# Optimization experiments

Measured on AMD Instinct MI355X. Metric: run time of the kernel, lower is better.

Reference implementation:

```python
import jax, jax.numpy as jnp
import numpy as np

B, C, H_IMG, W_IMG = 16, 384, 56, 56
NUM_HEADS = 6
HEAD_DIM = C // NUM_HEADS
BN_EPS = 1e-5


def _bn(x, gamma, beta, mean, var):
    # x: [b, ch, n] or [b, ch, h, w]; per-channel affine normalization (eval-mode BatchNorm)
    shape = (1, -1) + (1,) * (x.ndim - 2)
    scale = (gamma / jnp.sqrt(var + BN_EPS)).reshape(shape)
    shift = (beta - mean * gamma / jnp.sqrt(var + BN_EPS)).reshape(shape)
    return x * scale + shift


def setup_inputs() -> dict:
    key = jax.random.key(0)
    ks = jax.random.split(key, 12)
    c2 = 2 * C
    return {
        "x": jax.random.normal(ks[0], (B, C, H_IMG, W_IMG), jnp.float32),
        "qk_w": jax.random.normal(ks[1], (c2, C // 2), jnp.float32) * 0.05,
        "qk_gamma": jax.random.uniform(ks[2], (c2,), jnp.float32, 0.5, 1.5),
        "qk_beta": jax.random.normal(ks[3], (c2,), jnp.float32) * 0.1,
        "qk_mean": jax.random.normal(ks[4], (c2,), jnp.float32) * 0.1,
        "qk_var": jax.random.uniform(ks[5], (c2,), jnp.float32, 0.5, 1.5),
        "pe_w": jax.random.normal(ks[6], (C, 1, 3, 3), jnp.float32) * 0.1,
        "pe_gamma": jax.random.uniform(ks[7], (C,), jnp.float32, 0.5, 1.5),
        "pe_beta": jax.random.normal(ks[8], (C,), jnp.float32) * 0.1,
        "pe_mean": jax.random.normal(ks[9], (C,), jnp.float32) * 0.1,
        "pe_var": jax.random.uniform(ks[10], (C,), jnp.float32, 0.5, 1.5),
    }


def reference(x, qk_w, qk_gamma, qk_beta, qk_mean, qk_var,
              pe_w, pe_gamma, pe_beta, pe_mean, pe_var):
    b, c, h, w = x.shape
    n = h * w
    s = n ** (-0.5)
    nh, hd = NUM_HEADS, HEAD_DIM

    # grouped (groups=2) 1x1 conv: out channels [0:c] from input [0:c/2], [c:2c] from [c/2:c]
    xg = x.reshape(b, 2, c // 2, n)                       # [b, 2, c/2, n]
    wg = qk_w.reshape(2, c, c // 2)                       # [group, out_per_group, in_per_group]
    qk = jnp.einsum('bgin,goi->bgon', xg, wg).reshape(b, 2 * c, n)
    qk = _bn(qk, qk_gamma, qk_beta, qk_mean, qk_var)
    qk = jax.nn.elu(qk) + 1.0

    qk = qk.reshape(b, 2, nh, hd, n)
    q, k = qk[:, 0], qk[:, 1]                             # [b, H, d, n]
    v = x.reshape(b, nh, hd, n)                           # [b, H, d, n]

    # kv = (k*s) @ (v^T * s): [b, H, d, d]
    kv = jnp.einsum('bhdn,bhen->bhde', k * s, v * s)
    # numerator: q^T @ kv -> [b, H, n, d]
    num = jnp.einsum('bhdn,bhde->bhne', q, kv)
    # denominator: q^T @ mean_n(k) -> [b, H, n]
    den = jnp.einsum('bhdn,bhd->bhn', q, k.mean(axis=-1)) + 1e-6
    attn = (num / den[..., None]).transpose(0, 1, 3, 2).reshape(b, c, h, w)

    # depthwise 3x3 conv positional encoding on v (= x) + BN
    pe = jax.lax.conv_general_dilated(
        x, pe_w, window_strides=(1, 1), padding=((1, 1), (1, 1)),
        feature_group_count=c, dimension_numbers=('NCHW', 'OIHW', 'NCHW'))
    pe = _bn(pe, pe_gamma, pe_beta, pe_mean, pe_var)

    return attn + pe
```

## Files before the change

### kernel.cpp

```cpp
#include <hip/hip_runtime.h>
#include <math.h>

#define N_SP 3136
#define BN_EPS 1e-5f

typedef __attribute__((ext_vector_type(8))) short short8;
typedef __attribute__((ext_vector_type(4))) float f32x4;

#define K_SZ    (16*384*N_SP)
#define QB_OFF  (K_SZ)
#define QB_SZ   (16*384*N_SP)
#define KVP_OFF (QB_OFF + QB_SZ)
#define KVP_SZ  (16*6*7*64*80)
#define KVF_OFF (KVP_OFF + KVP_SZ)
#define KVF_SZ  (16*6*64*64)
#define KM_OFF  (KVF_OFF + KVF_SZ)
#define KM_SZ   (16*6*64)
#define WH_OFF  (KM_OFF + KM_SZ)
#define WSPLIT_N (2*384*192)
#define WF_G    (384*192)
#define PWS_OFF (WH_OFF + WSPLIT_N)
#define PSH_OFF (PWS_OFF + 384*9)

#define FSWZ(n) ((((n) >> 1) ^ ((n) >> 2)) & 7)

__device__ __forceinline__ void bsplit(float f, ushort& h, ushort& l) {
    uint u = __float_as_uint(f);
    uint hr = (u + 0x7FFFu + ((u >> 16) & 1u)) >> 16;
    h = (ushort)hr;
    float fh = __uint_as_float(hr << 16);
    float fl = f - fh;
    uint v = __float_as_uint(fl);
    l = (ushort)((v + 0x7FFFu + ((v >> 16) & 1u)) >> 16);
}

__global__ __launch_bounds__(256) void p0_prep(
    const float* __restrict__ qk_w, const float* __restrict__ pe_w,
    const float* __restrict__ pgamma, const float* __restrict__ pbeta,
    const float* __restrict__ pmean, const float* __restrict__ pvar,
    ushort* __restrict__ wfh, ushort* __restrict__ wfl,
    float* __restrict__ pwsc, float* __restrict__ psh)
{
    int idx = blockIdx.x * 256 + threadIdx.x;
    if (idx < WSPLIT_N) {
        int g = (idx >= WF_G) ? 1 : 0;
        int rem = idx - g * WF_G;
        int row = rem / 192, k = rem % 192;
        ushort h, l;
        bsplit(qk_w[idx], h, l);
        int dst = g * WF_G + ((row >> 4) * 24 + (k >> 3)) * 128 + (row & 15) * 8 + (k & 7);
        wfh[dst] = h;
        wfl[dst] = l;
    }
    if (idx < 384) {
        float sc = pgamma[idx] / sqrtf(pvar[idx] + BN_EPS);
        psh[idx] = pbeta[idx] - pmean[idx] * sc;
        #pragma unroll
        for (int q = 0; q < 9; ++q) pwsc[idx * 9 + q] = pe_w[idx * 9 + q] * sc;
    }
}

__global__ __launch_bounds__(256, 4) void k1_qk_mfma(
    const float* __restrict__ x, const ushort* __restrict__ wfh, const ushort* __restrict__ wfl,
    const float* __restrict__ gamma, const float* __restrict__ beta,
    const float* __restrict__ mean, const float* __restrict__ var,
    uint* __restrict__ kq, float* __restrict__ qbuf)
{
    __shared__ __align__(16) ushort Bh[4096];
    __shared__ __align__(16) ushort Bl[4096];
    __shared__ float scs[192], shs[192];

    const int bx = blockIdx.x;
    const int by = blockIdx.y;
    const int bz = blockIdx.z;
    const int b = bz >> 1, gg = bz & 1;
    const int t = threadIdx.x;
    const int lane = t & 63, wv = t >> 6;
    const int lg = lane >> 4, l15 = lane & 15;

    f32x4 acc[3][4];
    #pragma unroll
    for (int mf = 0; mf < 3; ++mf)
        #pragma unroll
        for (int nf = 0; nf < 4; ++nf)
            acc[mf][nf] = (f32x4){0.f, 0.f, 0.f, 0.f};

    const float* xg = x + (size_t)(b * 384 + gg * 192) * N_SP + bx * 64;
    const ushort* wfbh = wfh + gg * WF_G;
    const ushort* wfbl = wfl + gg * WF_G;

    for (int i = t; i < 192; i += 256) {
        int ch = gg * 384 + by * 192 + i;
        float sc = gamma[ch] / sqrtf(var[ch] + BN_EPS);
        scs[i] = sc;
        shs[i] = beta[ch] - mean[ch] * sc;
    }

    for (int kt = 0; kt < 3; ++kt) {
        #pragma unroll
        for (int li = 0; li < 2; ++li) {
            int idx = li * 256 + t;
            int kp = idx >> 4;
            int nq = idx & 15;
            int k0 = kp * 2;
            const float* px = xg + (size_t)(kt * 64 + k0) * N_SP + nq * 4;
            float4 v0 = *(const float4*)px;
            float4 v1 = *(const float4*)(px + N_SP);
            ushort h0[4], l0[4], h1[4], l1[4];
            float a0[4] = {v0.x, v0.y, v0.z, v0.w};
            float a1[4] = {v1.x, v1.y, v1.z, v1.w};
            #pragma unroll
            for (int i = 0; i < 4; ++i) { bsplit(a0[i], h0[i], l0[i]); bsplit(a1[i], h1[i], l1[i]); }
            int kb = k0 >> 3, ks = kp & 3;
            #pragma unroll
            for (int i = 0; i < 4; ++i) {
                int n = nq * 4 + i;
                int chunk = n * 8 + (kb ^ FSWZ(n));
                ((uint*)Bh)[chunk * 4 + ks] = (uint)h0[i] | ((uint)h1[i] << 16);
                ((uint*)Bl)[chunk * 4 + ks] = (uint)l0[i] | ((uint)l1[i] << 16);
            }
        }
        __syncthreads();
        #pragma unroll
        for (int s = 0; s < 2; ++s) {
            int kbq = s * 4 + lg;
            int kglob = kt * 8 + kbq;
            short8 bh[4], bl[4];
            #pragma unroll
            for (int nf = 0; nf < 4; ++nf) {
                int n = nf * 16 + l15;
                int chunk = n * 8 + (kbq ^ FSWZ(n));
                bh[nf] = *(const short8*)&Bh[chunk * 8];
                bl[nf] = *(const short8*)&Bl[chunk * 8];
            }
            #pragma unroll
            for (int mf = 0; mf < 3; ++mf) {
                int rb = by * 12 + wv * 3 + mf;
                int off = (rb * 24 + kglob) * 128 + l15 * 8;
                short8 ah = *(const short8*)&wfbh[off];
                short8 al = *(const short8*)&wfbl[off];
                #pragma unroll
                for (int nf = 0; nf < 4; ++nf) {
                    acc[mf][nf] = __builtin_amdgcn_mfma_f32_16x16x32_bf16(ah, bh[nf], acc[mf][nf], 0, 0, 0);
                    acc[mf][nf] = __builtin_amdgcn_mfma_f32_16x16x32_bf16(ah, bl[nf], acc[mf][nf], 0, 0, 0);
                    acc[mf][nf] = __builtin_amdgcn_mfma_f32_16x16x32_bf16(al, bh[nf], acc[mf][nf], 0, 0, 0);
                }
            }
        }
        __syncthreads();
    }

    size_t obase = ((size_t)b * 384 + by * 192) * N_SP + bx * 64;
    if (gg == 0) {
        #pragma unroll
        for (int mf = 0; mf < 3; ++mf)
            #pragma unroll
            for (int nf = 0; nf < 4; ++nf) {
                #pragma unroll
                for (int r = 0; r < 4; ++r) {
                    int lrow = wv * 48 + mf * 16 + lg * 4 + r;
                    float v = acc[mf][nf][r] * scs[lrow] + shs[lrow];
                    v = v > 0.f ? v + 1.f : __expf(v);
                    qbuf[obase + (size_t)lrow * N_SP + nf * 16 + l15] = v;
                }
            }
    } else {
        #pragma unroll
        for (int mf = 0; mf < 3; ++mf)
            #pragma unroll
            for (int nf = 0; nf < 4; ++nf) {
                #pragma unroll
                for (int r = 0; r < 4; ++r) {
                    int lrow = wv * 48 + mf * 16 + lg * 4 + r;
                    float v = acc[mf][nf][r] * scs[lrow] + shs[lrow];
                    v = v > 0.f ? v + 1.f : __expf(v);
                    ushort hh, ll;
                    bsplit(v, hh, ll);
                    kq[obase + (size_t)lrow * N_SP + nf * 16 + l15] = (uint)hh | ((uint)ll << 16);
                }
            }
    }
}

__global__ __launch_bounds__(256) void k2_kv_mfma(
    const float* __restrict__ x, const uint* __restrict__ kq,
    float* __restrict__ kv_part)
{
    __shared__ __align__(16) ushort Kh[4096], Kl[4096];
    __shared__ __align__(16) ushort Vh[5120], Vl[5120];

    const int chunk = blockIdx.x;
    const int h = blockIdx.y, b = blockIdx.z;
    const int t = threadIdx.x;
    const int lane = t & 63, wv = t >> 6;
    const int lg = lane >> 4, l15 = lane & 15;

    const uint* kp  = kq + (size_t)(b*384 + h*64) * N_SP;
    const float* vp = x  + (size_t)(b*384 + h*64) * N_SP;

    #pragma unroll
    for (int li = 0; li < 4; ++li) {
        int idx = li * 256 + t;
        int row = 64 + (idx >> 6), col = idx & 63;
        int off = (row * 8 + ((col >> 3) ^ (row & 7))) * 8 + (col & 7);
        Vh[off] = (row == 64) ? (ushort)0x3F80 : (ushort)0;
        Vl[off] = 0;
    }

    f32x4 acc[5];
    #pragma unroll
    for (int nf = 0; nf < 5; ++nf) acc[nf] = (f32x4){0.f, 0.f, 0.f, 0.f};

    for (int sub = 0; sub < 7; ++sub) {
        int n0 = chunk * 448 + sub * 64;
        #pragma unroll
        for (int li = 0; li < 4; ++li) {
            int idx = li * 256 + t;
            int row = idx >> 4, sc = idx & 15;
            int off = (row * 8 + ((sc >> 1) ^ (row & 7))) * 8 + (sc & 1) * 4;
            uint4 kf = *(const uint4*)&kp[(size_t)row * N_SP + n0 + sc * 4];
            ((uint*)&Kh[off])[0] = (kf.x & 0xFFFFu) | (kf.y << 16);
            ((uint*)&Kh[off])[1] = (kf.z & 0xFFFFu) | (kf.w << 16);
            ((uint*)&Kl[off])[0] = (kf.x >> 16) | (kf.y & 0xFFFF0000u);
            ((uint*)&Kl[off])[1] = (kf.z >> 16) | (kf.w & 0xFFFF0000u);
            float4 vf = *(const float4*)&vp[(size_t)row * N_SP + n0 + sc * 4];
            ushort h0,h1,h2,h3,l0,l1,l2,l3;
            bsplit(vf.x,h0,l0); bsplit(vf.y,h1,l1); bsplit(vf.z,h2,l2); bsplit(vf.w,h3,l3);
            ((uint*)&Vh[off])[0] = (uint)h0 | ((uint)h1 << 16);
            ((uint*)&Vh[off])[1] = (uint)h2 | ((uint)h3 << 16);
            ((uint*)&Vl[off])[0] = (uint)l0 | ((uint)l1 << 16);
            ((uint*)&Vl[off])[1] = (uint)l2 | ((uint)l3 << 16);
        }
        __syncthreads();
        #pragma unroll
        for (int s = 0; s < 2; ++s) {
            int arow = wv * 16 + l15;
            int akb = (s * 4 + lg) ^ (arow & 7);
            short8 ah = *(const short8*)&Kh[(arow * 8 + akb) * 8];
            short8 al = *(const short8*)&Kl[(arow * 8 + akb) * 8];
            #pragma unroll
            for (int nf = 0; nf < 5; ++nf) {
                int brow = nf * 16 + l15;
                int bkb = (s * 4 + lg) ^ (brow & 7);
                short8 bh = *(const short8*)&Vh[(brow * 8 + bkb) * 8];
                short8 bl = *(const short8*)&Vl[(brow * 8 + bkb) * 8];
                acc[nf] = __builtin_amdgcn_mfma_f32_16x16x32_bf16(ah, bh, acc[nf], 0, 0, 0);
                acc[nf] = __builtin_amdgcn_mfma_f32_16x16x32_bf16(ah, bl, acc[nf], 0, 0, 0);
                acc[nf] = __builtin_amdgcn_mfma_f32_16x16x32_bf16(al, bh, acc[nf], 0, 0, 0);
            }
        }
        __syncthreads();
    }

    size_t base = (size_t)((b*6 + h)*7 + chunk) * 64 * 80;
    #pragma unroll
    for (int nf = 0; nf < 5; ++nf)
        #pragma unroll
        for (int r = 0; r < 4; ++r) {
            int d = wv * 16 + lg * 4 + r;
            kv_part[base + (size_t)d * 80 + nf * 16 + l15] = acc[nf][r];
        }
}

__global__ __launch_bounds__(256) void k2b_reduce(
    const float* __restrict__ kv_part,
    float* __restrict__ kvf, float* __restrict__ km)
{
    const int bh = blockIdx.x;
    const int t = threadIdx.x;
    const float inv_n = 1.0f / (float)N_SP;
    const float* base = kv_part + (size_t)bh * 7 * 5120;
    float s[20];
    #pragma unroll
    for (int j = 0; j < 20; ++j) s[j] = 0.f;
    for (int c = 0; c < 7; ++c) {
        #pragma unroll
        for (int j = 0; j < 20; ++j) s[j] += base[c * 5120 + j * 256 + t];
    }
    #pragma unroll
    for (int j = 0; j < 20; ++j) {
        int i = j * 256 + t;
        int d = i / 80, e = i % 80;
        float v = s[j] * inv_n;
        if (e < 64)       kvf[(size_t)bh * 4096 + d * 64 + e] = v;
        else if (e == 64) km[bh * 64 + d] = v;
    }
}

__global__ __launch_bounds__(256) void k3_attn_pe(
    const float* __restrict__ x, const float* __restrict__ qbuf,
    const float* __restrict__ kvf, const float* __restrict__ km,
    const float* __restrict__ pwsc, const float* __restrict__ psh,
    float* __restrict__ out)
{
    __shared__ float qs[64][68];
    __shared__ float kms[64];
    const int bx = blockIdx.x;
    const int h = blockIdx.y, b = blockIdx.z;
    const int t = threadIdx.x, tx = t & 15, ty = t >> 4;
    const int n0 = bx * 64;
    const float* qp  = qbuf + (size_t)(b * 384 + h * 64) * N_SP;
    const float* kvp = kvf + (size_t)(b * 6 + h) * 4096;
    #pragma unroll
    for (int l = 0; l < 4; ++l) {
        int idx = t + l * 256;
        int d = idx >> 4, c = idx & 15;
        *(float4*)&qs[d][c * 4] = *(const float4*)&qp[(size_t)d * N_SP + n0 + c * 4];
    }
    if (t < 64) kms[t] = km[(b * 6 + h) * 64 + t];
    __syncthreads();

    float acc[4][4] = {};
    float den[4] = {};
    #pragma unroll 8
    for (int d = 0; d < 64; ++d) {
        float4 qn = *(const float4*)&qs[d][tx * 4];
        float4 ke = *(const float4*)&kvp[d * 64 + ty * 4];
        float qq[4] = {qn.x, qn.y, qn.z, qn.w}, kk[4] = {ke.x, ke.y, ke.z, ke.w};
        float kmd = kms[d];
        #pragma unroll
        for (int p = 0; p < 4; ++p) {
            den[p] += qq[p] * kmd;
            #pragma unroll
            for (int j = 0; j < 4; ++j) acc[p][j] += qq[p] * kk[j];
        }
    }

    const int p0 = n0 + tx * 4;
    const int y = p0 / 56, xc = p0 % 56;
    #pragma unroll
    for (int j = 0; j < 4; ++j) {
        int c = h * 64 + ty * 4 + j;
        const float* xp = x + ((size_t)b * 384 + c) * N_SP;
        float s6[3][6];
        #pragma unroll
        for (int dy = 0; dy < 3; ++dy) {
            int yy = y + dy - 1;
            bool yok = (yy >= 0) && (yy < 56);
            float4 mid = make_float4(0.f, 0.f, 0.f, 0.f);
            float lf = 0.f, rt = 0.f;
            if (yok) {
                const float* xr = xp + yy * 56;
                mid = *(const float4*)&xr[xc];
                if (xc > 0)  lf = xr[xc - 1];
                if (xc < 52) rt = xr[xc + 4];
            }
            s6[dy][0] = lf;  s6[dy][1] = mid.x; s6[dy][2] = mid.y;
            s6[dy][3] = mid.z; s6[dy][4] = mid.w; s6[dy][5] = rt;
        }
        float w9[9];
        #pragma unroll
        for (int q = 0; q < 9; ++q) w9[q] = pwsc[c * 9 + q];
        float sh2 = psh[c];
        float4 r;
        float* pr = (float*)&r;
        #pragma unroll
        for (int p = 0; p < 4; ++p) {
            float conv = 0.f;
            #pragma unroll
            for (int dy = 0; dy < 3; ++dy)
                #pragma unroll
                for (int dx = 0; dx < 3; ++dx)
                    conv += w9[dy * 3 + dx] * s6[dy][p + dx];
            pr[p] = acc[p][j] / (den[p] + 1e-6f) + conv + sh2;
        }
        *(float4*)&out[((size_t)b * 384 + c) * N_SP + p0] = r;
    }
}

extern "C" void kernel_launch(void* const* d_in, const int* in_sizes, int n_in,
                              void* d_out, int out_size, void* d_ws, size_t ws_size,
                              hipStream_t stream)
{
    const float* x        = (const float*)d_in[0];
    const float* qk_w     = (const float*)d_in[1];
    const float* qk_gamma = (const float*)d_in[2];
    const float* qk_beta  = (const float*)d_in[3];
    const float* qk_mean  = (const float*)d_in[4];
    const float* qk_var   = (const float*)d_in[5];
    const float* pe_w     = (const float*)d_in[6];
    const float* pe_gamma = (const float*)d_in[7];
    const float* pe_beta  = (const float*)d_in[8];
    const float* pe_mean  = (const float*)d_in[9];
    const float* pe_var   = (const float*)d_in[10];
    float* out = (float*)d_out;

    float* ws      = (float*)d_ws;
    uint* kq       = (uint*)ws;
    float* qbuf    = ws + QB_OFF;
    float* kv_part = ws + KVP_OFF;
    float* kvf     = ws + KVF_OFF;
    float* km      = ws + KM_OFF;
    ushort* wfh    = (ushort*)(ws + WH_OFF);
    ushort* wfl    = wfh + WSPLIT_N;
    float* pwsc    = ws + PWS_OFF;
    float* psh     = ws + PSH_OFF;

    hipLaunchKernelGGL(p0_prep, dim3((WSPLIT_N + 255)/256), dim3(256), 0, stream,
                       qk_w, pe_w, pe_gamma, pe_beta, pe_mean, pe_var,
                       wfh, wfl, pwsc, psh);
    dim3 g1(49, 2, 32);
    hipLaunchKernelGGL(k1_qk_mfma, g1, dim3(256), 0, stream,
                       x, wfh, wfl, qk_gamma, qk_beta, qk_mean, qk_var, kq, qbuf);
    dim3 g2(7, 6, 16);
    hipLaunchKernelGGL(k2_kv_mfma, g2, dim3(256), 0, stream, x, kq, kv_part);
    hipLaunchKernelGGL(k2b_reduce, dim3(96), dim3(256), 0, stream,
                       kv_part, kvf, km);
    dim3 g3(49, 6, 16);
    hipLaunchKernelGGL(k3_attn_pe, g3, dim3(256), 0, stream,
                       x, qbuf, kvf, km, pwsc, psh, out);
}
```

Baseline: 215.6 us.

## Fuse Q projection into attention kernel, dropping the Q intermediate buffer

The Q half of the grouped 1x1 conv is no longer computed in k1 and written to a global fp32 buffer. k3 now recomputes Q per tile with split-bf16 MFMAs, applies BN and ELU+1 into the shared tile, and then runs the attention and positional-encoding math. This removes a 77MB write and reread of Q. It adds x loads and MFMA work inside k3, and the shared tile is reused as staging space. The BN scale and shift for Q are precomputed in the prep kernel.

```diff
diff --git a/kernel.cpp b/kernel.cpp
--- a/kernel.cpp
+++ b/kernel.cpp
@@ -8,9 +8,7 @@
 typedef __attribute__((ext_vector_type(4))) float f32x4;
 
 #define K_SZ    (16*384*N_SP)
-#define QB_OFF  (K_SZ)
-#define QB_SZ   (16*384*N_SP)
-#define KVP_OFF (QB_OFF + QB_SZ)
+#define KVP_OFF (K_SZ)
 #define KVP_SZ  (16*6*7*64*80)
 #define KVF_OFF (KVP_OFF + KVP_SZ)
 #define KVF_SZ  (16*6*64*64)
@@ -21,6 +19,8 @@
 #define WF_G    (384*192)
 #define PWS_OFF (WH_OFF + WSPLIT_N)
 #define PSH_OFF (PWS_OFF + 384*9)
+#define QSC_OFF (PSH_OFF + 384)
+#define QSH_OFF (QSC_OFF + 384)
 
 #define FSWZ(n) ((((n) >> 1) ^ ((n) >> 2)) & 7)
 
@@ -36,10 +36,13 @@
 
 __global__ __launch_bounds__(256) void p0_prep(
     const float* __restrict__ qk_w, const float* __restrict__ pe_w,
+    const float* __restrict__ qk_gamma, const float* __restrict__ qk_beta,
+    const float* __restrict__ qk_mean, const float* __restrict__ qk_var,
     const float* __restrict__ pgamma, const float* __restrict__ pbeta,
     const float* __restrict__ pmean, const float* __restrict__ pvar,
     ushort* __restrict__ wfh, ushort* __restrict__ wfl,
-    float* __restrict__ pwsc, float* __restrict__ psh)
+    float* __restrict__ pwsc, float* __restrict__ psh,
+    float* __restrict__ qsc, float* __restrict__ qsh)
 {
     int idx = blockIdx.x * 256 + threadIdx.x;
     if (idx < WSPLIT_N) {
@@ -57,14 +60,17 @@
         psh[idx] = pbeta[idx] - pmean[idx] * sc;
         #pragma unroll
         for (int q = 0; q < 9; ++q) pwsc[idx * 9 + q] = pe_w[idx * 9 + q] * sc;
-    }
-}
-
-__global__ __launch_bounds__(256, 4) void k1_qk_mfma(
+        float qs = qk_gamma[idx] / sqrtf(qk_var[idx] + BN_EPS);
+        qsc[idx] = qs;
+        qsh[idx] = qk_beta[idx] - qk_mean[idx] * qs;
+    }
+}
+
+__global__ __launch_bounds__(256, 4) void k1_k_mfma(
     const float* __restrict__ x, const ushort* __restrict__ wfh, const ushort* __restrict__ wfl,
     const float* __restrict__ gamma, const float* __restrict__ beta,
     const float* __restrict__ mean, const float* __restrict__ var,
-    uint* __restrict__ kq, float* __restrict__ qbuf)
+    uint* __restrict__ kq)
 {
     __shared__ __align__(16) ushort Bh[4096];
     __shared__ __align__(16) ushort Bl[4096];
@@ -72,8 +78,7 @@
 
     const int bx = blockIdx.x;
     const int by = blockIdx.y;
-    const int bz = blockIdx.z;
-    const int b = bz >> 1, gg = bz & 1;
+    const int b = blockIdx.z;
     const int t = threadIdx.x;
     const int lane = t & 63, wv = t >> 6;
     const int lg = lane >> 4, l15 = lane & 15;
@@ -85,12 +90,12 @@
         for (int nf = 0; nf < 4; ++nf)
             acc[mf][nf] = (f32x4){0.f, 0.f, 0.f, 0.f};
 
-    const float* xg = x + (size_t)(b * 384 + gg * 192) * N_SP + bx * 64;
-    const ushort* wfbh = wfh + gg * WF_G;
-    const ushort* wfbl = wfl + gg * WF_G;
+    const float* xg = x + (size_t)(b * 384 + 192) * N_SP + bx * 64;
+    const ushort* wfbh = wfh + WF_G;
+    const ushort* wfbl = wfl + WF_G;
 
     for (int i = t; i < 192; i += 256) {
-        int ch = gg * 384 + by * 192 + i;
+        int ch = 384 + by * 192 + i;
         float sc = gamma[ch] / sqrtf(var[ch] + BN_EPS);
         scs[i] = sc;
         shs[i] = beta[ch] - mean[ch] * sc;
@@ -110,14 +115,14 @@
             float a0[4] = {v0.x, v0.y, v0.z, v0.w};
             float a1[4] = {v1.x, v1.y, v1.z, v1.w};
             #pragma unroll
-            for (int i = 0; i < 4; ++i) { bsplit(a0[i], h0[i], l0[i]); bsplit(a1[i], h1[i], l1[i]); }
+            for (int i2 = 0; i2 < 4; ++i2) { bsplit(a0[i2], h0[i2], l0[i2]); bsplit(a1[i2], h1[i2], l1[i2]); }
             int kb = k0 >> 3, ks = kp & 3;
             #pragma unroll
-            for (int i = 0; i < 4; ++i) {
-                int n = nq * 4 + i;
+            for (int i2 = 0; i2 < 4; ++i2) {
+                int n = nq * 4 + i2;
                 int chunk = n * 8 + (kb ^ FSWZ(n));
-                ((uint*)Bh)[chunk * 4 + ks] = (uint)h0[i] | ((uint)h1[i] << 16);
-                ((uint*)Bl)[chunk * 4 + ks] = (uint)l0[i] | ((uint)l1[i] << 16);
+                ((uint*)Bh)[chunk * 4 + ks] = (uint)h0[i2] | ((uint)h1[i2] << 16);
+                ((uint*)Bl)[chunk * 4 + ks] = (uint)l0[i2] | ((uint)l1[i2] << 16);
             }
         }
         __syncthreads();
@@ -151,35 +156,20 @@
     }
 
     size_t obase = ((size_t)b * 384 + by * 192) * N_SP + bx * 64;
-    if (gg == 0) {
-        #pragma unroll
-        for (int mf = 0; mf < 3; ++mf)
-            #pragma unroll
-            for (int nf = 0; nf < 4; ++nf) {
-                #pragma unroll
-                for (int r = 0; r < 4; ++r) {
-                    int lrow = wv * 48 + mf * 16 + lg * 4 + r;
-                    float v = acc[mf][nf][r] * scs[lrow] + shs[lrow];
-                    v = v > 0.f ? v + 1.f : __expf(v);
-                    qbuf[obase + (size_t)lrow * N_SP + nf * 16 + l15] = v;
-                }
-            }
-    } else {
-        #pragma unroll
-        for (int mf = 0; mf < 3; ++mf)
-            #pragma unroll
-            for (int nf = 0; nf < 4; ++nf) {
-                #pragma unroll
-                for (int r = 0; r < 4; ++r) {
-                    int lrow = wv * 48 + mf * 16 + lg * 4 + r;
-                    float v = acc[mf][nf][r] * scs[lrow] + shs[lrow];
-                    v = v > 0.f ? v + 1.f : __expf(v);
-                    ushort hh, ll;
-                    bsplit(v, hh, ll);
-                    kq[obase + (size_t)lrow * N_SP + nf * 16 + l15] = (uint)hh | ((uint)ll << 16);
-                }
-            }
-    }
+    #pragma unroll
+    for (int mf = 0; mf < 3; ++mf)
+        #pragma unroll
+        for (int nf = 0; nf < 4; ++nf) {
+            #pragma unroll
+            for (int r = 0; r < 4; ++r) {
+                int lrow = wv * 48 + mf * 16 + lg * 4 + r;
+                float v = acc[mf][nf][r] * scs[lrow] + shs[lrow];
+                v = v > 0.f ? v + 1.f : __expf(v);
+                ushort hh, ll;
+                bsplit(v, hh, ll);
+                kq[obase + (size_t)lrow * N_SP + nf * 16 + l15] = (uint)hh | ((uint)ll << 16);
+            }
+        }
 }
 
 __global__ __launch_bounds__(256) void k2_kv_mfma(
@@ -288,28 +278,109 @@
 }
 
 __global__ __launch_bounds__(256) void k3_attn_pe(
-    const float* __restrict__ x, const float* __restrict__ qbuf,
+    const float* __restrict__ x,
+    const ushort* __restrict__ wfh, const ushort* __restrict__ wfl,
+    const float* __restrict__ qsc, const float* __restrict__ qsh,
     const float* __restrict__ kvf, const float* __restrict__ km,
     const float* __restrict__ pwsc, const float* __restrict__ psh,
     float* __restrict__ out)
 {
     __shared__ float qs[64][68];
     __shared__ float kms[64];
+    ushort* Bh = (ushort*)&qs[0][0];
+    ushort* Bl = Bh + 4096;
+
     const int bx = blockIdx.x;
     const int h = blockIdx.y, b = blockIdx.z;
-    const int t = threadIdx.x, tx = t & 15, ty = t >> 4;
+    const int t = threadIdx.x;
+    const int lane = t & 63, wv = t >> 6;
+    const int lg = lane >> 4, l15 = lane & 15;
     const int n0 = bx * 64;
-    const float* qp  = qbuf + (size_t)(b * 384 + h * 64) * N_SP;
-    const float* kvp = kvf + (size_t)(b * 6 + h) * 4096;
-    #pragma unroll
-    for (int l = 0; l < 4; ++l) {
-        int idx = t + l * 256;
-        int d = idx >> 4, c = idx & 15;
-        *(float4*)&qs[d][c * 4] = *(const float4*)&qp[(size_t)d * N_SP + n0 + c * 4];
+
+    const float* xg = x + (size_t)b * 384 * N_SP + n0;
+    const ushort* wfbh = wfh;
+    const ushort* wfbl = wfl;
+
+    f32x4 qacc[4];
+    #pragma unroll
+    for (int nf = 0; nf < 4; ++nf) qacc[nf] = (f32x4){0.f, 0.f, 0.f, 0.f};
+
+    for (int kt = 0; kt < 3; ++kt) {
+        #pragma unroll
+        for (int li = 0; li < 2; ++li) {
+            int idx = li * 256 + t;
+            int kp = idx >> 4;
+            int nq = idx & 15;
+            int k0 = kp * 2;
+            const float* px = xg + (size_t)(kt * 64 + k0) * N_SP + nq * 4;
+            float4 v0 = *(const float4*)px;
+            float4 v1 = *(const float4*)(px + N_SP);
+            ushort h0[4], l0[4], h1[4], l1[4];
+            float a0[4] = {v0.x, v0.y, v0.z, v0.w};
+            float a1[4] = {v1.x, v1.y, v1.z, v1.w};
+            #pragma unroll
+            for (int i = 0; i < 4; ++i) { bsplit(a0[i], h0[i], l0[i]); bsplit(a1[i], h1[i], l1[i]); }
+            int kb = k0 >> 3, ks = kp & 3;
+            #pragma unroll
+            for (int i = 0; i < 4; ++i) {
+                int n = nq * 4 + i;
+                int chunk = n * 8 + (kb ^ FSWZ(n));
+                ((uint*)Bh)[chunk * 4 + ks] = (uint)h0[i] | ((uint)h1[i] << 16);
+                ((uint*)Bl)[chunk * 4 + ks] = (uint)l0[i] | ((uint)l1[i] << 16);
+            }
+        }
+        __syncthreads();
+        #pragma unroll
+        for (int s = 0; s < 2; ++s) {
+            int kbq = s * 4 + lg;
+            int kglob = kt * 8 + kbq;
+            short8 bh[4], bl[4];
+            #pragma unroll
+            for (int nf = 0; nf < 4; ++nf) {
+                int n = nf * 16 + l15;
+                int chunk = n * 8 + (kbq ^ FSWZ(n));
+                bh[nf] = *(const short8*)&Bh[chunk * 8];
+                bl[nf] = *(const short8*)&Bl[chunk * 8];
+            }
+            int rb = h * 4 + wv;
+            int off = (rb * 24 + kglob) * 128 + l15 * 8;
+            short8 ah = *(const short8*)&wfbh[off];
+            short8 al = *(const short8*)&wfbl[off];
+            #pragma unroll
+            for (int nf = 0; nf < 4; ++nf) {
+                qacc[nf] = __builtin_amdgcn_mfma_f32_16x16x32_bf16(ah, bh[nf], qacc[nf], 0, 0, 0);
+                qacc[nf] = __builtin_amdgcn_mfma_f32_16x16x32_bf16(ah, bl[nf], qacc[nf], 0, 0, 0);
+                qacc[nf] = __builtin_amdgcn_mfma_f32_16x16x32_bf16(al, bh[nf], qacc[nf], 0, 0, 0);
+            }
+        }
+        __syncthreads();
+    }
+
+    {
+        float sc4[4], sh4[4];
+        #pragma unroll
+        for (int r = 0; r < 4; ++r) {
+            int ch = h * 64 + wv * 16 + lg * 4 + r;
+            sc4[r] = qsc[ch];
+            sh4[r] = qsh[ch];
+        }
+        #pragma unroll
+        for (int nf = 0; nf < 4; ++nf) {
+            int col = nf * 16 + l15;
+            #pragma unroll
+            for (int r = 0; r < 4; ++r) {
+                int row = wv * 16 + lg * 4 + r;
+                float v = qacc[nf][r] * sc4[r] + sh4[r];
+                v = v > 0.f ? v + 1.f : __expf(v);
+                qs[row][col] = v;
+            }
+        }
     }
     if (t < 64) kms[t] = km[(b * 6 + h) * 64 + t];
     __syncthreads();
 
+    const int tx = t & 15, ty = t >> 4;
+    const float* kvp = kvf + (size_t)(b * 6 + h) * 4096;
     float acc[4][4] = {};
     float den[4] = {};
     #pragma unroll 8
@@ -387,7 +458,6 @@
 
     float* ws      = (float*)d_ws;
     uint* kq       = (uint*)ws;
-    float* qbuf    = ws + QB_OFF;
     float* kv_part = ws + KVP_OFF;
     float* kvf     = ws + KVF_OFF;
     float* km      = ws + KM_OFF;
@@ -395,18 +465,21 @@
     ushort* wfl    = wfh + WSPLIT_N;
     float* pwsc    = ws + PWS_OFF;
     float* psh     = ws + PSH_OFF;
+    float* qsc     = ws + QSC_OFF;
+    float* qsh     = ws + QSH_OFF;
 
     hipLaunchKernelGGL(p0_prep, dim3((WSPLIT_N + 255)/256), dim3(256), 0, stream,
-                       qk_w, pe_w, pe_gamma, pe_beta, pe_mean, pe_var,
-                       wfh, wfl, pwsc, psh);
-    dim3 g1(49, 2, 32);
-    hipLaunchKernelGGL(k1_qk_mfma, g1, dim3(256), 0, stream,
-                       x, wfh, wfl, qk_gamma, qk_beta, qk_mean, qk_var, kq, qbuf);
+                       qk_w, pe_w, qk_gamma, qk_beta, qk_mean, qk_var,
+                       pe_gamma, pe_beta, pe_mean, pe_var,
+                       wfh, wfl, pwsc, psh, qsc, qsh);
+    dim3 g1(49, 2, 16);
+    hipLaunchKernelGGL(k1_k_mfma, g1, dim3(256), 0, stream,
+                       x, wfh, wfl, qk_gamma, qk_beta, qk_mean, qk_var, kq);
     dim3 g2(7, 6, 16);
     hipLaunchKernelGGL(k2_kv_mfma, g2, dim3(256), 0, stream, x, kq, kv_part);
     hipLaunchKernelGGL(k2b_reduce, dim3(96), dim3(256), 0, stream,
                        kv_part, kvf, km);
     dim3 g3(49, 6, 16);
     hipLaunchKernelGGL(k3_attn_pe, g3, dim3(256), 0, stream,
-                       x, qbuf, kvf, km, pwsc, psh, out);
-}
+                       x, wfh, wfl, qsc, qsh, kvf, km, pwsc, psh, out);
+}
```

Result: faster. 208.2 us (median of 2 runs) (-3.5%).
